# Optimization experiments

Measured on AMD Instinct MI355X. Metric: run time of the kernel, lower is better.

## Reference

```python
import jax, jax.numpy as jnp
import numpy as np

P = 7            # cfg.POOLING_SIZE (= group_size)
N_CLASSES = 21   # PASCAL VOC incl. background
SPATIAL_SCALE = 1.0 / 16.0


def _round_half_up(x):
    # matches C round() for non-negative roi coords (jnp.round is banker's)
    return jnp.floor(x + 0.5)


def psroi_pool(feat, rois, out_dim):
    """Position-sensitive RoI average pooling via integral images.
    feat: [B, out_dim*P*P, H, W]; rois: [N, 5] (batch_idx, x1, y1, x2, y2).
    Returns [N, out_dim, P, P]."""
    B, C, H, W = feat.shape
    # summed-area table, zero-padded: S[b,c,h,w] = sum feat[b,c,:h,:w]
    S = jnp.cumsum(jnp.cumsum(feat, axis=2), axis=3)
    S = jnp.pad(S, ((0, 0), (0, 0), (1, 0), (1, 0)))

    b = rois[:, 0].astype(jnp.int32)
    x1 = _round_half_up(rois[:, 1]) * SPATIAL_SCALE
    y1 = _round_half_up(rois[:, 2]) * SPATIAL_SCALE
    x2 = _round_half_up(rois[:, 3] + 1.0) * SPATIAL_SCALE
    y2 = _round_half_up(rois[:, 4] + 1.0) * SPATIAL_SCALE
    roi_w = jnp.maximum(x2 - x1, 0.1)
    roi_h = jnp.maximum(y2 - y1, 0.1)
    bin_w = roi_w / P
    bin_h = roi_h / P

    g = jnp.arange(P, dtype=feat.dtype)
    hs = jnp.clip(jnp.floor(g[None] * bin_h[:, None] + y1[:, None]), 0, H).astype(jnp.int32)        # [N,P]
    he = jnp.clip(jnp.ceil((g[None] + 1.0) * bin_h[:, None] + y1[:, None]), 0, H).astype(jnp.int32)
    ws = jnp.clip(jnp.floor(g[None] * bin_w[:, None] + x1[:, None]), 0, W).astype(jnp.int32)
    we = jnp.clip(jnp.ceil((g[None] + 1.0) * bin_w[:, None] + x1[:, None]), 0, W).astype(jnp.int32)

    # channel for (ctop, gh, gw) is (ctop*P + gh)*P + gw == arange(C) reshaped
    c = jnp.arange(C, dtype=jnp.int32).reshape(1, out_dim, P, P)
    bi = b[:, None, None, None]
    h0 = hs[:, None, :, None]; h1 = he[:, None, :, None]
    w0 = ws[:, None, None, :]; w1 = we[:, None, None, :]
    # box-sum from integral image -> [N, out_dim, P, P]
    ssum = S[bi, c, h1, w1] - S[bi, c, h0, w1] - S[bi, c, h1, w0] + S[bi, c, h0, w0]

    dh = jnp.maximum(he - hs, 0)[:, None, :, None]
    dw = jnp.maximum(we - ws, 0)[:, None, None, :]
    area = (dh * dw).astype(feat.dtype)
    return jnp.where(area > 0, ssum / jnp.maximum(area, 1.0), 0.0)


def setup_inputs() -> dict:
    key = jax.random.key(0)
    k1, k2, k3, k4, k5 = jax.random.split(key, 5)
    B, Cin, H, W = 4, 2048, 64, 64
    base_feat = jax.random.normal(k1, (B, Cin, H, W), jnp.float32)
    w_conv1 = 0.01 * jax.random.normal(k2, (1024, Cin), jnp.float32)
    w_cls = 0.01 * jax.random.normal(k3, (N_CLASSES * P * P, 1024), jnp.float32)
    w_bbox = 0.001 * jax.random.normal(k4, (4 * N_CLASSES * P * P, 1024), jnp.float32)
    # 300 ROIs per image in image coords (image size = 16*H = 1024)
    n_per = 300
    ka, kb = jax.random.split(k5)
    xy1 = jax.random.uniform(ka, (B * n_per, 2), jnp.float32, 0.0, 900.0)
    wh = jax.random.uniform(kb, (B * n_per, 2), jnp.float32, 16.0, 160.0)
    xy2 = jnp.minimum(xy1 + wh, 1023.0)
    bidx = jnp.repeat(jnp.arange(B, dtype=jnp.float32), n_per)[:, None]
    rois = jnp.concatenate([bidx, xy1[:, 0:1], xy1[:, 1:2], xy2[:, 0:1], xy2[:, 1:2]], axis=1)
    return {"base_feat": base_feat, "rois": rois, "w_conv1": w_conv1, "w_cls": w_cls, "w_bbox": w_bbox}


def reference(base_feat, rois, w_conv1, w_cls, w_bbox):
    B = base_feat.shape[0]
    n_per = rois.shape[0] // B
    # 1x1 conv (no bias) + relu
    x = jax.nn.relu(jnp.einsum('oi,bihw->bohw', w_conv1, base_feat))
    # cls branch: 1x1 conv -> PSRoIPool -> PxP avgpool -> softmax
    cls_feat = jnp.einsum('oi,bihw->bohw', w_cls, x)
    pooled_cls = psroi_pool(cls_feat, rois, N_CLASSES)        # [N, 21, P, P]
    cls_score = pooled_cls.mean(axis=(2, 3))                   # [N, 21]
    cls_prob = jax.nn.softmax(cls_score, axis=1)
    # bbox branch: 1x1 conv -> PSRoIPool -> PxP avgpool
    bbox_feat = jnp.einsum('oi,bihw->bohw', w_bbox, x)
    pooled_loc = psroi_pool(bbox_feat, rois, 4 * N_CLASSES)    # [N, 84, P, P]
    bbox_pred = pooled_loc.mean(axis=(2, 3))                    # [N, 84]
    return cls_prob.reshape(B, n_per, -1), bbox_pred.reshape(B, n_per, -1)
```

## Files before the change

kernel.cpp:

```cpp
#include <hip/hip_runtime.h>
#include <cstdint>


typedef __attribute__((ext_vector_type(8))) short short8;
typedef __attribute__((ext_vector_type(4))) short short4v;
typedef __attribute__((ext_vector_type(4))) float f32x4;

#define OFF_FEATT 0ull
#define OFF_W1    67108864ull
#define OFF_X     71303168ull
#define OFF_WC    104857600ull
#define OFF_DESC  117702656ull
#define OFF_P     0ull

__device__ __forceinline__ unsigned short f2bf(float f) {
  unsigned u = __float_as_uint(f);
  u += 0x7fffu + ((u >> 16) & 1u);
  return (unsigned short)(u >> 16);
}
__device__ __forceinline__ float bf2f(unsigned short h) {
  return __uint_as_float(((unsigned)h) << 16);
}

__device__ __forceinline__ int swz6(int k6, int key) {
  return ((((k6 >> 3) & 7) ^ key) << 3) | (k6 & 7);
}

__device__ __forceinline__ void gload16(const void* g, void* l) {
  __builtin_amdgcn_global_load_lds((const __attribute__((address_space(1))) void*)g,
                                   (__attribute__((address_space(3))) void*)l, 16, 0, 0);
}

__global__ __launch_bounds__(256) void k_prep(const float* __restrict__ w_conv1,
                                              const float* __restrict__ wcls,
                                              const float* __restrict__ wbbox,
                                              const float* __restrict__ rois,
                                              const float* __restrict__ base_feat,
                                              unsigned short* __restrict__ w1b,
                                              unsigned short* __restrict__ Wc,
                                              int* __restrict__ desc,
                                              unsigned short* __restrict__ featT) {
  __shared__ float tile[64][65];
  int bid = blockIdx.x;
  if (bid < 2048) {
    int t = bid * 256 + threadIdx.x;
    long e = (long)t * 4;
    int o = (int)(e >> 11), k = (int)(e & 2047);
    float4 q = *(const float4*)(w_conv1 + e);
    short4v s = {(short)f2bf(q.x), (short)f2bf(q.y), (short)f2bf(q.z), (short)f2bf(q.w)};
    int kp = (k & ~63) | swz6(k & 63, o & 7);
    *(short4v*)(w1b + (size_t)o * 2048 + kp) = s;
  } else if (bid < 8320) {
    int t = (bid - 2048) * 256 + threadIdx.x;
    size_t e = (size_t)t * 4;
    int c = (int)(e / 50176);
    int rem = (int)(e - (size_t)c * 50176);
    int ij = rem >> 10, k = rem & 1023;
    float4 q = make_float4(0.f, 0.f, 0.f, 0.f);
    if (c < 21)       q = *(const float4*)(wcls + (size_t)(c * 49 + ij) * 1024 + k);
    else if (c < 105) q = *(const float4*)(wbbox + (size_t)((c - 21) * 49 + ij) * 1024 + k);
    short4v s = {(short)f2bf(q.x), (short)f2bf(q.y), (short)f2bf(q.z), (short)f2bf(q.w)};
    int kp = (k & ~63) | swz6(k & 63, c & 7);
    *(short4v*)(Wc + ((size_t)(c * 49 + ij) * 1024 + kp)) = s;
  } else if (bid < 8565) {
    int t = (bid - 8320) * 256 + threadIdx.x;
    if (t >= 1280 * 49) return;
    int roi = t / 49, ij = t - roi * 49;
    int* d = desc + (size_t)t * 8;
    if (roi >= 1200) { d[0] = 0; d[1] = 0; d[2] = 0; d[3] = 0; d[4] = 0; ((float*)d)[5] = 0.f; return; }
    const float* r = rois + (size_t)roi * 5;
    int b = (int)r[0];
    float x1 = __fmul_rn(floorf(__fadd_rn(r[1], 0.5f)), 0.0625f);
    float y1 = __fmul_rn(floorf(__fadd_rn(r[2], 0.5f)), 0.0625f);
    float x2 = __fmul_rn(floorf(__fadd_rn(__fadd_rn(r[3], 1.0f), 0.5f)), 0.0625f);
    float y2 = __fmul_rn(floorf(__fadd_rn(__fadd_rn(r[4], 1.0f), 0.5f)), 0.0625f);
    float bw = __fdiv_rn(fmaxf(__fsub_rn(x2, x1), 0.1f), 7.0f);
    float bh = __fdiv_rn(fmaxf(__fsub_rn(y2, y1), 0.1f), 7.0f);
    int i = ij / 7, j = ij - (ij / 7) * 7;
    float fi = (float)i, fj = (float)j;
    int hs = (int)fminf(fmaxf(floorf(__fadd_rn(__fmul_rn(fi, bh), y1)), 0.f), 64.f);
    int he = (int)fminf(fmaxf(ceilf(__fadd_rn(__fmul_rn(__fadd_rn(fi, 1.f), bh), y1)), 0.f), 64.f);
    int wsx = (int)fminf(fmaxf(floorf(__fadd_rn(__fmul_rn(fj, bw), x1)), 0.f), 64.f);
    int we = (int)fminf(fmaxf(ceilf(__fadd_rn(__fmul_rn(__fadd_rn(fj, 1.f), bw), x1)), 0.f), 64.f);
    int dh = max(he - hs, 0), dw = max(we - wsx, 0);
    float inv = (dh * dw > 0) ? 1.0f / (float)(dh * dw) : 0.f;
    d[0] = b; d[1] = hs; d[2] = he; d[3] = wsx; d[4] = we;
    ((float*)d)[5] = inv;
  } else {
    int t = bid - 8565;
    int s0 = (t & 63) * 64;
    int c0 = ((t >> 6) & 31) * 64;
    int b = t >> 11;
    int tx = threadIdx.x & 63, ty = threadIdx.x >> 6;
    const float* sp = base_feat + ((size_t)b * 2048 + c0) * 4096 + s0;
#pragma unroll
    for (int i = 0; i < 16; i++) {
      int cl = ty * 16 + i;
      tile[cl][tx] = sp[(size_t)cl * 4096 + tx];
    }
    __syncthreads();
    unsigned short* dp = featT + ((size_t)b * 4096 + s0) * 2048 + c0;
    int c4 = (threadIdx.x & 15) * 4;
    int sy = threadIdx.x >> 4;
#pragma unroll
    for (int i = 0; i < 4; i++) {
      int sl = i * 16 + sy;
      int key = sl & 7;
      short4v v = {(short)f2bf(tile[c4 + 0][sl]), (short)f2bf(tile[c4 + 1][sl]),
                   (short)f2bf(tile[c4 + 2][sl]), (short)f2bf(tile[c4 + 3][sl])};
      *(short4v*)(dp + (size_t)sl * 2048 + swz6(c4, key)) = v;
    }
  }
}

__global__ __launch_bounds__(256) void k_gemm_conv1(const short* __restrict__ A,
                                                    const short* __restrict__ Bw,
                                                    unsigned short* __restrict__ X) {
  int mt = blockIdx.x, nt = blockIdx.y, b = blockIdx.z;
  __shared__ short As[128 * 64];
  __shared__ short Bs[128 * 64];
  int tid = threadIdx.x, lane = tid & 63, wave = tid >> 6;
  int wm = wave >> 1, wn = wave & 1;
  f32x4 acc[4][4];
#pragma unroll
  for (int i = 0; i < 4; i++)
#pragma unroll
    for (int j = 0; j < 4; j++) acc[i][j] = (f32x4){0.f, 0.f, 0.f, 0.f};

  const short* Ab = A + ((size_t)b * 4096 + (size_t)mt * 128) * 2048;
  const short* Bb = Bw + (size_t)nt * 128 * 2048;
  int lr = lane >> 3;
  int lc = (lane & 7) * 8;
  int key = lane & 7;

  for (int k0 = 0; k0 < 2048; k0 += 64) {
#pragma unroll
    for (int i = 0; i < 4; i++) {
      int row = i * 32 + wave * 8 + lr;
      gload16(Ab + (size_t)row * 2048 + k0 + lc, (char*)As + (i * 32 + wave * 8) * 128);
      gload16(Bb + (size_t)row * 2048 + k0 + lc, (char*)Bs + (i * 32 + wave * 8) * 128);
    }
    __syncthreads();
#pragma unroll
    for (int kt = 0; kt < 2; kt++) {
      int ko = (((kt << 2) | (lane >> 4)) ^ key) << 3;
      short8 af[4], bfr[4];
#pragma unroll
      for (int i = 0; i < 4; i++)
        af[i] = *(const short8*)(As + (wm * 64 + i * 16 + (lane & 15)) * 64 + ko);
#pragma unroll
      for (int j = 0; j < 4; j++)
        bfr[j] = *(const short8*)(Bs + (wn * 64 + j * 16 + (lane & 15)) * 64 + ko);
#pragma unroll
      for (int i = 0; i < 4; i++)
#pragma unroll
        for (int j = 0; j < 4; j++)
          acc[i][j] = __builtin_amdgcn_mfma_f32_16x16x32_bf16(af[i], bfr[j], acc[i][j], 0, 0, 0);
    }
    __syncthreads();
  }
  unsigned short* Xo = X + ((size_t)b * 4096 + (size_t)mt * 128) * 1024 + nt * 128;
#pragma unroll
  for (int i = 0; i < 4; i++)
#pragma unroll
    for (int j = 0; j < 4; j++) {
      int row = wm * 64 + i * 16 + (lane >> 4) * 4;
      int col = wn * 64 + j * 16 + (lane & 15);
#pragma unroll
      for (int r = 0; r < 4; r++)
        Xo[(size_t)(row + r) * 1024 + col] = f2bf(fmaxf(acc[i][j][r], 0.f));
    }
}

__global__ __launch_bounds__(256) void k_fusedpool(const unsigned short* __restrict__ Xb,
                                                   const int* __restrict__ desc,
                                                   const unsigned short* __restrict__ Wc,
                                                   unsigned short* __restrict__ P,
                                                   int nroi) {
  int mt = blockIdx.x;
  int ij = blockIdx.y;
  int kh = blockIdx.z;
  __shared__ short As[64 * 64];
  __shared__ short Bs[128 * 64];
  __shared__ int dsc[64][4];
  int tid = threadIdx.x, lane = tid & 63, wave = tid >> 6;

  if (tid < 64) {
    const int* d = desc + ((size_t)(mt * 64 + tid) * 49 + ij) * 8;
    int b = d[0], hs = d[1], he = d[2], wsx = d[3], we = d[4];
    dsc[tid][0] = (b * 64 + hs) * 64 + wsx;
    dsc[tid][1] = max(he - hs, 0);
    dsc[tid][2] = max(we - wsx, 0);
    dsc[tid][3] = d[5];
  }
  __syncthreads();

  f32x4 acc[4][2];
#pragma unroll
  for (int i = 0; i < 4; i++)
#pragma unroll
    for (int j = 0; j < 2; j++) acc[i][j] = (f32x4){0.f, 0.f, 0.f, 0.f};

  const unsigned short* Bb = Wc + (size_t)ij * 1024;
  int lr = lane >> 3, lc = (lane & 7) * 8;
  int key = lane & 7;
  int r8 = tid >> 3;
  int k8 = tid & 7;

  int kbeg = kh * 512, kend = kbeg + 512;
  for (int k0 = kbeg; k0 < kend; k0 += 64) {
#pragma unroll
    for (int i = 0; i < 4; i++) {
      int row = i * 32 + wave * 8 + lr;
      gload16(Bb + (size_t)row * (49 * 1024) + k0 + lc, (char*)Bs + (i * 32 + wave * 8) * 128);
    }
#pragma unroll 1
    for (int p = 0; p < 2; p++) {
      int r = p * 32 + r8;
      int cs = dsc[r][0], dh = dsc[r][1], dw = dsc[r][2];
      float inv = __int_as_float(dsc[r][3]);
      const unsigned short* xp = Xb + (size_t)cs * 1024 + k0 + k8 * 8;
      float a0 = 0.f, a1 = 0.f, a2 = 0.f, a3 = 0.f;
      float a4 = 0.f, a5 = 0.f, a6 = 0.f, a7 = 0.f;
#pragma unroll
      for (int hh = 0; hh < 3; hh++) {
#pragma unroll
        for (int ww = 0; ww < 3; ww++) {
          int ho = (hh < dh) ? hh : 0;
          int wo = (ww < dw) ? ww : 0;
          float m = ((hh < dh) && (ww < dw)) ? inv : 0.f;
          short8 v = *(const short8*)(xp + (size_t)(ho * 64 + wo) * 1024);
          a0 = fmaf(m, bf2f((unsigned short)v[0]), a0);
          a1 = fmaf(m, bf2f((unsigned short)v[1]), a1);
          a2 = fmaf(m, bf2f((unsigned short)v[2]), a2);
          a3 = fmaf(m, bf2f((unsigned short)v[3]), a3);
          a4 = fmaf(m, bf2f((unsigned short)v[4]), a4);
          a5 = fmaf(m, bf2f((unsigned short)v[5]), a5);
          a6 = fmaf(m, bf2f((unsigned short)v[6]), a6);
          a7 = fmaf(m, bf2f((unsigned short)v[7]), a7);
        }
      }
      short8 o = {(short)f2bf(a0), (short)f2bf(a1), (short)f2bf(a2), (short)f2bf(a3),
                  (short)f2bf(a4), (short)f2bf(a5), (short)f2bf(a6), (short)f2bf(a7)};
      *(short8*)(As + r * 64 + ((k8 ^ (r & 7)) << 3)) = o;
    }
    __syncthreads();
#pragma unroll
    for (int kt = 0; kt < 2; kt++) {
      int ko = (((kt << 2) | (lane >> 4)) ^ key) << 3;
      short8 af[4], bfr[2];
#pragma unroll
      for (int i = 0; i < 4; i++)
        af[i] = *(const short8*)(As + (i * 16 + (lane & 15)) * 64 + ko);
#pragma unroll
      for (int j = 0; j < 2; j++)
        bfr[j] = *(const short8*)(Bs + (wave * 32 + j * 16 + (lane & 15)) * 64 + ko);
#pragma unroll
      for (int i = 0; i < 4; i++)
#pragma unroll
        for (int j = 0; j < 2; j++)
          acc[i][j] = __builtin_amdgcn_mfma_f32_16x16x32_bf16(af[i], bfr[j], acc[i][j], 0, 0, 0);
    }
    __syncthreads();
  }
  unsigned short* Pb = P + (size_t)(kh * 49 + ij) * nroi * 112;
#pragma unroll
  for (int i = 0; i < 4; i++)
#pragma unroll
    for (int j = 0; j < 2; j++) {
      int cc = wave * 32 + j * 16 + (lane & 15);
      if (cc < 112) {
        int rbase = mt * 64 + i * 16 + (lane >> 4) * 4;
#pragma unroll
        for (int r = 0; r < 4; r++)
          Pb[(size_t)(rbase + r) * 112 + cc] = f2bf(acc[i][j][r]);
      }
    }
}

__global__ __launch_bounds__(128) void k_redfinal(const unsigned short* __restrict__ P,
                                                  float* __restrict__ out, int nroi) {
  int roi = blockIdx.x;
  int c = threadIdx.x;
  __shared__ float sc[112];
  __shared__ float es[32];
  if (c < 112) {
    const unsigned short* p = P + (size_t)roi * 112 + c;
    float s = 0.f;
#pragma unroll 7
    for (int ij = 0; ij < 98; ij++) s += bf2f(p[(size_t)ij * nroi * 112]);
    sc[c] = s * (1.f / 49.f);
  }
  __syncthreads();
  if (c < 21) {
    float mx = -1e30f;
#pragma unroll
    for (int k = 0; k < 21; k++) mx = fmaxf(mx, sc[k]);
    es[c] = expf(sc[c] - mx);
  }
  __syncthreads();
  if (c < 21) {
    float sum = 0.f;
#pragma unroll
    for (int k = 0; k < 21; k++) sum += es[k];
    float rs = 1.f / sum;
    out[(size_t)roi * 21 + c] = es[c] * rs;
  }
  if (c >= 21 && c < 105) {
    out[25200 + (size_t)roi * 84 + (c - 21)] = sc[c];
  }
}

extern "C" void kernel_launch(void* const* d_in, const int* in_sizes, int n_in,
                              void* d_out, int out_size, void* d_ws, size_t ws_size,
                              hipStream_t stream) {
  const float* base_feat = (const float*)d_in[0];
  const float* rois      = (const float*)d_in[1];
  const float* w_conv1   = (const float*)d_in[2];
  const float* w_cls     = (const float*)d_in[3];
  const float* w_bbox    = (const float*)d_in[4];
  float* out = (float*)d_out;
  char* ws = (char*)d_ws;

  unsigned short* featT = (unsigned short*)(ws + OFF_FEATT);
  unsigned short* w1b   = (unsigned short*)(ws + OFF_W1);
  unsigned short* X     = (unsigned short*)(ws + OFF_X);
  unsigned short* Wc    = (unsigned short*)(ws + OFF_WC);
  int*            desc  = (int*)(ws + OFF_DESC);
  unsigned short* P     = (unsigned short*)(ws + OFF_P);

  k_prep<<<16757, 256, 0, stream>>>(w_conv1, w_cls, w_bbox, rois, base_feat,
                                    w1b, Wc, desc, featT);
  k_gemm_conv1<<<dim3(32, 8, 4), 256, 0, stream>>>((const short*)featT, (const short*)w1b, X);
  k_fusedpool<<<dim3(20, 49, 2), 256, 0, stream>>>(X, desc, Wc, P, 1280);
  k_redfinal<<<1200, 128, 0, stream>>>(P, out, 1280);
}
```

Before: 377.8 us.

## Rewrite conv1 GEMM with 256x256 tiles and multi-stage LDS pipeline

The 1x1 conv GEMM moves from 128x128 tiles with 256 threads and synchronous load-then-compute to 256x256 tiles with 512 threads. A 9-slot LDS ring buffer is filled by async global-to-LDS loads issued several half-tiles ahead, guarded by explicit vmcnt waits and raw barriers. MFMA blocks are interleaved with the staging and run at raised wave priority. This is meant to hide global memory latency and raise arithmetic intensity, at the cost of fragile hand-tuned waitcnt ordering, heavy LDS use (144 KB), and fewer blocks (256) for occupancy.

```diff
diff --git a/kernel.cpp b/kernel.cpp
--- a/kernel.cpp
+++ b/kernel.cpp
@@ -113,62 +113,118 @@
   }
 }
 
-__global__ __launch_bounds__(256) void k_gemm_conv1(const short* __restrict__ A,
-                                                    const short* __restrict__ Bw,
-                                                    unsigned short* __restrict__ X) {
-  int mt = blockIdx.x, nt = blockIdx.y, b = blockIdx.z;
-  __shared__ short As[128 * 64];
-  __shared__ short Bs[128 * 64];
+__global__ __launch_bounds__(512, 2) void k_gemm_conv1(const short* __restrict__ A,
+                                                       const short* __restrict__ Bw,
+                                                       unsigned short* __restrict__ X) {
+  __shared__ short lds[9 * 8192];
+  int mt = blockIdx.x, nt = blockIdx.y;
   int tid = threadIdx.x, lane = tid & 63, wave = tid >> 6;
-  int wm = wave >> 1, wn = wave & 1;
-  f32x4 acc[4][4];
-#pragma unroll
-  for (int i = 0; i < 4; i++)
+  int wm = wave >> 2, wn = wave & 3;
+
+  const short* Ab = A + (size_t)mt * 256 * 2048;
+  const short* Bb = Bw + (size_t)nt * 256 * 2048;
+
+  f32x4 acc[8][4];
+#pragma unroll
+  for (int i = 0; i < 8; i++)
 #pragma unroll
     for (int j = 0; j < 4; j++) acc[i][j] = (f32x4){0.f, 0.f, 0.f, 0.f};
 
-  const short* Ab = A + ((size_t)b * 4096 + (size_t)mt * 128) * 2048;
-  const short* Bb = Bw + (size_t)nt * 128 * 2048;
-  int lr = lane >> 3;
-  int lc = (lane & 7) * 8;
+  int sr = tid >> 3;
+  int sc = (tid & 7) * 8;
+  auto stage_half = [&](int h) {
+    if (h >= 128) return;
+    int kind = h & 3, tl = h >> 2, slot = h % 9;
+    const short* src = ((kind & 2) ? Bb : Ab)
+                     + (size_t)((kind & 1) * 128 + sr) * 2048 + tl * 64 + sc;
+    char* dst = (char*)lds + slot * 16384 + tid * 16;
+    gload16(src, dst);
+    gload16(src + (size_t)64 * 2048, dst + 8192);
+  };
+
+#pragma unroll
+  for (int h = 0; h < 5; h++) stage_half(h);
+
+  int la15 = lane & 15;
   int key = lane & 7;
-
-  for (int k0 = 0; k0 < 2048; k0 += 64) {
-#pragma unroll
-    for (int i = 0; i < 4; i++) {
-      int row = i * 32 + wave * 8 + lr;
-      gload16(Ab + (size_t)row * 2048 + k0 + lc, (char*)As + (i * 32 + wave * 8) * 128);
-      gload16(Bb + (size_t)row * 2048 + k0 + lc, (char*)Bs + (i * 32 + wave * 8) * 128);
-    }
-    __syncthreads();
-#pragma unroll
-    for (int kt = 0; kt < 2; kt++) {
-      int ko = (((kt << 2) | (lane >> 4)) ^ key) << 3;
-      short8 af[4], bfr[4];
-#pragma unroll
-      for (int i = 0; i < 4; i++)
-        af[i] = *(const short8*)(As + (wm * 64 + i * 16 + (lane & 15)) * 64 + ko);
+  int ko0 = (((lane >> 4)) ^ key) << 3;
+  int ko1 = ((4 | (lane >> 4)) ^ key) << 3;
+  int bro = (wn & 1) * 64;
+
+  for (int t = 0; t < 32; ++t) {
+    if (t < 31) asm volatile("s_waitcnt vmcnt(2)" ::: "memory");
+    else        asm volatile("s_waitcnt vmcnt(0)" ::: "memory");
+    __builtin_amdgcn_s_barrier();
+    __builtin_amdgcn_sched_barrier(0);
+    const short* Asl = lds + (size_t)((4 * t + wm) % 9) * 8192;
+    const short* Bsl = lds + (size_t)((4 * t + 2 + (wn >> 1)) % 9) * 8192;
+    short8 af[4], bf[4];
+
+    stage_half(4 * t + 5);
+#pragma unroll
+    for (int j = 0; j < 4; j++)
+      bf[j] = *(const short8*)(Bsl + (bro + j * 16 + la15) * 64 + ko0);
+#pragma unroll
+    for (int i = 0; i < 4; i++)
+      af[i] = *(const short8*)(Asl + (i * 16 + la15) * 64 + ko0);
+    __builtin_amdgcn_s_setprio(1);
+#pragma unroll
+    for (int i = 0; i < 4; i++)
 #pragma unroll
       for (int j = 0; j < 4; j++)
-        bfr[j] = *(const short8*)(Bs + (wn * 64 + j * 16 + (lane & 15)) * 64 + ko);
-#pragma unroll
-      for (int i = 0; i < 4; i++)
-#pragma unroll
-        for (int j = 0; j < 4; j++)
-          acc[i][j] = __builtin_amdgcn_mfma_f32_16x16x32_bf16(af[i], bfr[j], acc[i][j], 0, 0, 0);
-    }
-    __syncthreads();
-  }
-  unsigned short* Xo = X + ((size_t)b * 4096 + (size_t)mt * 128) * 1024 + nt * 128;
-#pragma unroll
-  for (int i = 0; i < 4; i++)
+        acc[i][j] = __builtin_amdgcn_mfma_f32_16x16x32_bf16(af[i], bf[j], acc[i][j], 0, 0, 0);
+    __builtin_amdgcn_s_setprio(0);
+
+    stage_half(4 * t + 6);
+#pragma unroll
+    for (int i = 0; i < 4; i++)
+      af[i] = *(const short8*)(Asl + (64 + i * 16 + la15) * 64 + ko0);
+    __builtin_amdgcn_s_setprio(1);
+#pragma unroll
+    for (int i = 0; i < 4; i++)
+#pragma unroll
+      for (int j = 0; j < 4; j++)
+        acc[4 + i][j] = __builtin_amdgcn_mfma_f32_16x16x32_bf16(af[i], bf[j], acc[4 + i][j], 0, 0, 0);
+    __builtin_amdgcn_s_setprio(0);
+
+    stage_half(4 * t + 7);
+#pragma unroll
+    for (int j = 0; j < 4; j++)
+      bf[j] = *(const short8*)(Bsl + (bro + j * 16 + la15) * 64 + ko1);
+#pragma unroll
+    for (int i = 0; i < 4; i++)
+      af[i] = *(const short8*)(Asl + (i * 16 + la15) * 64 + ko1);
+    __builtin_amdgcn_s_setprio(1);
+#pragma unroll
+    for (int i = 0; i < 4; i++)
+#pragma unroll
+      for (int j = 0; j < 4; j++)
+        acc[i][j] = __builtin_amdgcn_mfma_f32_16x16x32_bf16(af[i], bf[j], acc[i][j], 0, 0, 0);
+    __builtin_amdgcn_s_setprio(0);
+
+    stage_half(4 * t + 8);
+#pragma unroll
+    for (int i = 0; i < 4; i++)
+      af[i] = *(const short8*)(Asl + (64 + i * 16 + la15) * 64 + ko1);
+    __builtin_amdgcn_s_setprio(1);
+#pragma unroll
+    for (int i = 0; i < 4; i++)
+#pragma unroll
+      for (int j = 0; j < 4; j++)
+        acc[4 + i][j] = __builtin_amdgcn_mfma_f32_16x16x32_bf16(af[i], bf[j], acc[4 + i][j], 0, 0, 0);
+    __builtin_amdgcn_s_setprio(0);
+  }
+
+  unsigned short* Xo = X + ((size_t)(mt * 256 + wm * 128)) * 1024 + nt * 256 + wn * 64;
+#pragma unroll
+  for (int ii = 0; ii < 8; ii++)
 #pragma unroll
     for (int j = 0; j < 4; j++) {
-      int row = wm * 64 + i * 16 + (lane >> 4) * 4;
-      int col = wn * 64 + j * 16 + (lane & 15);
+      int row = ii * 16 + (lane >> 4) * 4;
+      int col = j * 16 + la15;
 #pragma unroll
       for (int r = 0; r < 4; r++)
-        Xo[(size_t)(row + r) * 1024 + col] = f2bf(fmaxf(acc[i][j][r], 0.f));
+        Xo[(size_t)(row + r) * 1024 + col] = f2bf(fmaxf(acc[ii][j][r], 0.f));
     }
 }
 
@@ -331,7 +387,7 @@
 
   k_prep<<<16757, 256, 0, stream>>>(w_conv1, w_cls, w_bbox, rois, base_feat,
                                     w1b, Wc, desc, featT);
-  k_gemm_conv1<<<dim3(32, 8, 4), 256, 0, stream>>>((const short*)featT, (const short*)w1b, X);
+  k_gemm_conv1<<<dim3(64, 4), 512, 0, stream>>>((const short*)featT, (const short*)w1b, X);
   k_fusedpool<<<dim3(20, 49, 2), 256, 0, stream>>>(X, desc, Wc, P, 1280);
   k_redfinal<<<1200, 128, 0, stream>>>(P, out, 1280);
 }
```

Result: faster. 356.0 us (-5.7%).
